# Optimization experiments

Measured on AMD Instinct MI355X. Metric: run time of the kernel, lower is better.

## Reference

```python
import jax, jax.numpy as jnp
import numpy as np

SEQ_LEN = 4096
EMBED_DIM = 2048
NUM_HEADS = 16
HEAD_DIM = EMBED_DIM // NUM_HEADS


def setup_inputs() -> dict:
    key = jax.random.key(0)
    k1, k2, k3 = jax.random.split(key, 3)
    x = jax.random.normal(k1, (SEQ_LEN, EMBED_DIM), dtype=jnp.float32)
    # Dense-layer params (lecun-normal-ish scaling for stability)
    W_qkv = jax.random.normal(k2, (EMBED_DIM, 3 * EMBED_DIM), dtype=jnp.float32) / np.sqrt(EMBED_DIM)
    b_qkv = jnp.zeros((3 * EMBED_DIM,), dtype=jnp.float32)
    W_out = jax.random.normal(k3, (EMBED_DIM, EMBED_DIM), dtype=jnp.float32) / np.sqrt(EMBED_DIM)
    b_out = jnp.zeros((EMBED_DIM,), dtype=jnp.float32)
    return {"x": x, "W_qkv": W_qkv, "b_qkv": b_qkv, "W_out": W_out, "b_out": b_out}


def reference(x, W_qkv, b_qkv, W_out, b_out):
    seq_len = x.shape[0]
    qkv = x @ W_qkv + b_qkv                       # (S, 3E)
    qkv = qkv.reshape(seq_len, 3, NUM_HEADS, HEAD_DIM)
    q, k, v = qkv[:, 0], qkv[:, 1], qkv[:, 2]     # each (S, H, D)
    scale = 1.0 / jnp.sqrt(jnp.float32(HEAD_DIM))
    # NOTE: faithful to source -- contracts over BOTH heads and head_dim,
    # producing a single (S, S) attention matrix shared across heads.
    attn = jnp.einsum('thd,shd->ts', q, k) * scale
    causal = jnp.triu(jnp.ones((seq_len, seq_len), dtype=bool), k=1)
    attn = jnp.where(causal, -jnp.inf, attn)
    attn = jax.nn.softmax(attn, axis=-1)
    out = jnp.einsum('ts,shd->thd', attn, v)      # (S, H, D)
    out = out.reshape(seq_len, EMBED_DIM)
    return out @ W_out + b_out
```

## Files before the change

### kernel.cpp

```cpp
#include <hip/hip_runtime.h>
#include <cstdint>
#include <cstddef>

#define SEQLEN 4096
#define EMBED  2048
#define NH     16
#define HD     128
#define N3     6144
#define SCALE  0.08838834764831845f
#define MBIAS  25.0f
#define LB3    12288
#define LB1    8192

typedef __attribute__((ext_vector_type(8))) short bf16x8;
typedef __attribute__((ext_vector_type(4))) float f32x4;
typedef unsigned short u16;

#define MFMA(a, b, c) __builtin_amdgcn_mfma_f32_16x16x32_bf16((a), (b), (c), 0, 0, 0)

__device__ inline u16 f2bf(float f) {
  uint32_t u = __float_as_uint(f);
  u += 0x7FFF + ((u >> 16) & 1);
  return (u16)(u >> 16);
}

__device__ inline float bf2f(u16 u) {
  return __uint_as_float(((uint32_t)u) << 16);
}

__device__ inline void gload_lds16(const u16* g, u16* l) {
  __builtin_amdgcn_global_load_lds((const __attribute__((address_space(1))) void*)g,
                                   (__attribute__((address_space(3))) void*)l, 16, 0, 0);
}

__device__ __forceinline__ void stage3(const u16* a0, const u16* a1, const u16* b0,
                                       u16* base, int w, int lane) {
  gload_lds16(a0, base + w * 512 + lane * 8);
  gload_lds16(a1, base + 4096 + w * 512 + lane * 8);
  gload_lds16(b0, base + 8192 + w * 512 + lane * 8);
}

__device__ __forceinline__ void mm256x128(const u16* gA, size_t sA, const u16* gB, size_t sB,
                                          int NT, u16* lds, f32x4 (&acc)[4][4]) {
  int tid = threadIdx.x;
  int w = tid >> 6, lane = tid & 63;
  int g = lane >> 4, lr = lane & 15;
  int wm = w >> 1, wn = w & 1;
  int arow = (w << 4) + (lane >> 2);
  int cb = (((lane & 3) ^ (arow & 3)) << 3);
  const u16* a0 = gA + (size_t)arow * sA + cb;
  const u16* a1 = a0 + (size_t)128 * sA;
  const u16* b0 = gB + (size_t)arow * sB + cb;
  int gx = ((g ^ (lr & 3)) << 3);
  int aoff = ((wm << 6) + lr) * 32 + gx;
  int boff = 8192 + ((wn << 6) + lr) * 32 + gx;
  stage3(a0, a1, b0, lds, w, lane);
  stage3(a0 + 32, a1 + 32, b0 + 32, lds + LB3, w, lane);
  asm volatile("s_waitcnt vmcnt(3)" ::: "memory");
  __builtin_amdgcn_s_barrier();
  for (int t = 0; t < NT; ++t) {
    u16* base = lds + (t % 3) * LB3;
    bf16x8 af[4], bfr[4];
    #pragma unroll
    for (int m = 0; m < 4; m++) af[m] = *(const bf16x8*)(base + aoff + m * 512);
    #pragma unroll
    for (int n = 0; n < 4; n++) bfr[n] = *(const bf16x8*)(base + boff + n * 512);
    if (t + 2 < NT) {
      int kt = (t + 2) << 5;
      stage3(a0 + kt, a1 + kt, b0 + kt, lds + ((t + 2) % 3) * LB3, w, lane);
    }
    __builtin_amdgcn_s_setprio(1);
    #pragma unroll
    for (int m = 0; m < 4; m++)
      #pragma unroll
      for (int n = 0; n < 4; n++)
        acc[m][n] = MFMA(af[m], bfr[n], acc[m][n]);
    __builtin_amdgcn_s_setprio(0);
    if (t + 1 < NT) {
      if (t + 2 < NT) asm volatile("s_waitcnt vmcnt(3)" ::: "memory");
      else            asm volatile("s_waitcnt vmcnt(0)" ::: "memory");
      __builtin_amdgcn_s_barrier();
    }
  }
  asm volatile("" ::: "memory");
}

__device__ __forceinline__ void stage2h(const u16* a0, const u16* b0, u16* base, int w, int lane) {
  gload_lds16(a0, base + w * 512 + lane * 8);
  gload_lds16(b0, base + 4096 + w * 512 + lane * 8);
}

__device__ __forceinline__ void mm128x128(const u16* gA, size_t sA, const u16* gB, size_t sB,
                                          int NT, u16* lds, f32x4 (&acc)[4][2]) {
  int tid = threadIdx.x;
  int w = tid >> 6, lane = tid & 63;
  int g = lane >> 4, lr = lane & 15;
  int wm = w >> 2, wn = w & 3;
  int srow = lane >> 2;
  int cb = (((lane & 3) ^ (srow & 3)) << 3);
  const u16* a0 = gA + (size_t)((w << 4) + srow) * sA + cb;
  const u16* b0 = gB + (size_t)((w << 4) + srow) * sB + cb;
  int gx = ((g ^ (lr & 3)) << 3);
  int aoff = ((wm << 6) + lr) * 32 + gx;
  int boff = 4096 + ((wn << 5) + lr) * 32 + gx;
  stage2h(a0, b0, lds, w, lane);
  stage2h(a0 + 32, b0 + 32, lds + LB1, w, lane);
  asm volatile("s_waitcnt vmcnt(2)" ::: "memory");
  __builtin_amdgcn_s_barrier();
  for (int t = 0; t < NT; ++t) {
    u16* base = lds + (t % 3) * LB1;
    bf16x8 af[4], bfr[2];
    #pragma unroll
    for (int m = 0; m < 4; m++) af[m] = *(const bf16x8*)(base + aoff + m * 512);
    #pragma unroll
    for (int n = 0; n < 2; n++) bfr[n] = *(const bf16x8*)(base + boff + n * 512);
    if (t + 2 < NT) {
      int kt = (t + 2) << 5;
      stage2h(a0 + kt, b0 + kt, lds + ((t + 2) % 3) * LB1, w, lane);
    }
    __builtin_amdgcn_s_setprio(1);
    #pragma unroll
    for (int m = 0; m < 4; m++)
      #pragma unroll
      for (int n = 0; n < 2; n++)
        acc[m][n] = MFMA(af[m], bfr[n], acc[m][n]);
    __builtin_amdgcn_s_setprio(0);
    if (t + 1 < NT) {
      if (t + 2 < NT) asm volatile("s_waitcnt vmcnt(2)" ::: "memory");
      else            asm volatile("s_waitcnt vmcnt(0)" ::: "memory");
      __builtin_amdgcn_s_barrier();
    }
  }
  asm volatile("" ::: "memory");
}

__global__ __launch_bounds__(256) void conv_f32_bf16(const float* __restrict__ in,
                                                     u16* __restrict__ out, int n) {
  int i = (blockIdx.x * 256 + threadIdx.x) * 4;
  if (i >= n) return;
  float4 v = *(const float4*)(in + i);
  ushort4 o;
  o.x = f2bf(v.x); o.y = f2bf(v.y); o.z = f2bf(v.z); o.w = f2bf(v.w);
  *(ushort4*)(out + i) = o;
}

__global__ __launch_bounds__(256) void transpose_conv(const float* __restrict__ in,
                                                      u16* __restrict__ out, int R, int C) {
  __shared__ float t[32][33];
  int c0 = blockIdx.x * 32, r0 = blockIdx.y * 32;
  int tx = threadIdx.x, ty = threadIdx.y;
  #pragma unroll
  for (int i = ty; i < 32; i += 8)
    t[i][tx] = in[(size_t)(r0 + i) * C + c0 + tx];
  __syncthreads();
  #pragma unroll
  for (int i = ty; i < 32; i += 8)
    out[(size_t)(c0 + i) * R + r0 + tx] = f2bf(t[tx][i]);
}

__global__ __launch_bounds__(256) void vtrans(const u16* __restrict__ qkv, u16* __restrict__ vT) {
  __shared__ u16 t[32][33];
  int c0 = blockIdx.x * 32, t0 = blockIdx.y * 32;
  int tx = threadIdx.x, ty = threadIdx.y;
  #pragma unroll
  for (int i = ty; i < 32; i += 8)
    t[i][tx] = qkv[(size_t)(t0 + i) * N3 + 2 * EMBED + c0 + tx];
  __syncthreads();
  #pragma unroll
  for (int i = ty; i < 32; i += 8)
    vT[(size_t)(c0 + i) * SEQLEN + t0 + tx] = t[tx][i];
}

__global__ __launch_bounds__(512, 4) void gemm_bt2(const u16* __restrict__ A, const u16* __restrict__ Bt,
                                                   const float* __restrict__ bias,
                                                   u16* __restrict__ Cb, float* __restrict__ Cf,
                                                   int M, int N, int K, int out_f32) {
  __shared__ __align__(16) u16 lds[3 * LB3];
  int bn = blockIdx.x, bm = blockIdx.y;
  f32x4 acc[4][4] = {};
  mm256x128(A + (size_t)(bm * 256) * K, K, Bt + (size_t)(bn * 128) * K, K, K >> 5, lds, acc);
  int tid = threadIdx.x;
  int w = tid >> 6, lane = tid & 63, g = lane >> 4, lr = lane & 15;
  int wm = w >> 1, wn = w & 1;
  int r0 = bm * 256 + wm * 64, c0 = bn * 128 + wn * 64;
  #pragma unroll
  for (int n = 0; n < 4; n++) {
    int c = c0 + n * 16 + lr;
    float bv = bias[c];
    #pragma unroll
    for (int m = 0; m < 4; m++)
      #pragma unroll
      for (int j = 0; j < 4; j++) {
        int r = r0 + m * 16 + g * 4 + j;
        float v = acc[m][n][j] + bv;
        if (out_f32) Cf[(size_t)r * N + c] = v;
        else         Cb[(size_t)r * N + c] = f2bf(v);
      }
  }
}

__global__ __launch_bounds__(512, 4) void sgemm_p2(const u16* __restrict__ qkv,
                                                   u16* __restrict__ P) {
  int bx = blockIdx.x, by = blockIdx.y;
  int r0g = by * 256, c0g = bx * 128;
  if (c0g > r0g + 255) return;
  __shared__ __align__(16) u16 lds[3 * LB3];
  f32x4 acc[4][4] = {};
  mm256x128(qkv + (size_t)r0g * N3, N3, qkv + (size_t)c0g * N3 + EMBED, N3, EMBED >> 5, lds, acc);
  int tid = threadIdx.x;
  int w = tid >> 6, lane = tid & 63, g = lane >> 4, lr = lane & 15;
  int wm = w >> 1, wn = w & 1;
  int r0 = r0g + wm * 64, c0 = c0g + wn * 64;
  #pragma unroll
  for (int m = 0; m < 4; m++)
    #pragma unroll
    for (int n = 0; n < 4; n++) {
      int c = c0 + n * 16 + lr;
      #pragma unroll
      for (int j = 0; j < 4; j++) {
        int r = r0 + m * 16 + g * 4 + j;
        float p = (c <= r) ? __expf(fmaf(acc[m][n][j], SCALE, -MBIAS)) : 0.f;
        P[(size_t)r * SEQLEN + c] = f2bf(p);
      }
    }
}

__global__ __launch_bounds__(256) void psum(const u16* __restrict__ P, float* __restrict__ L) {
  int wave = threadIdx.x >> 6, lane = threadIdx.x & 63;
  int r = blockIdx.x * 4 + wave;
  int ctop = ((r >> 8) + 1) * 256;
  const u16* Prow = P + (size_t)r * SEQLEN;
  float s = 0.f;
  for (int c = lane * 8; c < ctop; c += 512) {
    bf16x8 v = *(const bf16x8*)(Prow + c);
    #pragma unroll
    for (int j = 0; j < 8; j++) s += bf2f((u16)v[j]);
  }
  s += __shfl_xor(s, 1);  s += __shfl_xor(s, 2);  s += __shfl_xor(s, 4);
  s += __shfl_xor(s, 8);  s += __shfl_xor(s, 16); s += __shfl_xor(s, 32);
  if (lane == 0) L[r] = s;
}

__global__ __launch_bounds__(512, 4) void pv_gemm3(const u16* __restrict__ P,
                                                   const u16* __restrict__ vT,
                                                   const float* __restrict__ L,
                                                   u16* __restrict__ O) {
  __shared__ __align__(16) u16 lds[3 * LB1];
  int bx = blockIdx.x, pp = blockIdx.y;
  int tid = threadIdx.x;
  int w = tid >> 6, lane = tid & 63, g = lane >> 4, lr = lane & 15;
  int wm = w >> 2, wn = w & 3;
  int c0g = bx * 128;
  #pragma unroll
  for (int pass = 0; pass < 2; pass++) {
    int rt = pass ? pp : (31 - pp);
    int r0g = rt * 128;
    int NT = (r0g + 128) >> 5;
    f32x4 acc[4][2] = {};
    mm128x128(P + (size_t)r0g * SEQLEN, SEQLEN, vT + (size_t)c0g * SEQLEN, SEQLEN, NT, lds, acc);
    int r0 = r0g + wm * 64, c0 = c0g + wn * 32;
    #pragma unroll
    for (int m = 0; m < 4; m++) {
      float invl[4];
      #pragma unroll
      for (int j = 0; j < 4; j++)
        invl[j] = 1.f / L[r0 + m * 16 + g * 4 + j];
      #pragma unroll
      for (int n = 0; n < 2; n++) {
        int c = c0 + n * 16 + lr;
        #pragma unroll
        for (int j = 0; j < 4; j++) {
          int r = r0 + m * 16 + g * 4 + j;
          O[(size_t)r * EMBED + c] = f2bf(acc[m][n][j] * invl[j]);
        }
      }
    }
    __syncthreads();
  }
}

extern "C" void kernel_launch(void* const* d_in, const int* in_sizes, int n_in,
                              void* d_out, int out_size, void* d_ws, size_t ws_size,
                              hipStream_t stream) {
  const float* x     = (const float*)d_in[0];
  const float* W_qkv = (const float*)d_in[1];
  const float* b_qkv = (const float*)d_in[2];
  const float* W_out = (const float*)d_in[3];
  const float* b_out = (const float*)d_in[4];
  float* out = (float*)d_out;

  u16* xb    = (u16*)d_ws;
  u16* qkvb  = xb + (size_t)SEQLEN * EMBED;
  u16* Pbuf  = qkvb + (size_t)SEQLEN * N3;
  u16* vT    = Pbuf + (size_t)SEQLEN * SEQLEN;
  float* Lbuf = (float*)(vT + (size_t)EMBED * SEQLEN);
  u16* attb  = xb;
  u16* WqkvT = Pbuf;
  u16* WoutT = Pbuf;

  conv_f32_bf16<<<SEQLEN * EMBED / 1024, 256, 0, stream>>>(x, xb, SEQLEN * EMBED);
  transpose_conv<<<dim3(N3 / 32, EMBED / 32), dim3(32, 8), 0, stream>>>(W_qkv, WqkvT, EMBED, N3);
  gemm_bt2<<<dim3(N3 / 128, SEQLEN / 256), 512, 0, stream>>>(xb, WqkvT, b_qkv, qkvb, nullptr,
                                                             SEQLEN, N3, EMBED, 0);
  vtrans<<<dim3(EMBED / 32, SEQLEN / 32), dim3(32, 8), 0, stream>>>(qkvb, vT);
  sgemm_p2<<<dim3(SEQLEN / 128, SEQLEN / 256), 512, 0, stream>>>(qkvb, Pbuf);
  psum<<<SEQLEN / 4, 256, 0, stream>>>(Pbuf, Lbuf);
  pv_gemm3<<<dim3(EMBED / 128, 16), 512, 0, stream>>>(Pbuf, vT, Lbuf, attb);
  transpose_conv<<<dim3(EMBED / 32, EMBED / 32), dim3(32, 8), 0, stream>>>(W_out, WoutT, EMBED, EMBED);
  gemm_bt2<<<dim3(EMBED / 128, SEQLEN / 256), 512, 0, stream>>>(attb, WoutT, b_out, nullptr, out,
                                                                SEQLEN, EMBED, EMBED, 1);
}
```

Before: 318.2 us.

## Use 4-wave 256x128 GEMM tiles and fuse softmax row sums into score kernel

Adds a 256-thread GEMM mainloop in which each wave computes a 128x64 sub-tile (8x4 MFMA accumulators), giving more register reuse per LDS load. The QKV projection and the score kernel both use it. The score kernel also reduces exp values per row in registers and writes partial sums to a small buffer. A tiny kernel then sums those partials, replacing the pass that re-read the whole P matrix. The trade-offs are higher register pressure with fewer waves per block, plus an added memset and partial-sum buffer.

```diff
diff --git a/kernel.cpp b/kernel.cpp
--- a/kernel.cpp
+++ b/kernel.cpp
@@ -10,6 +10,7 @@
 #define SCALE  0.08838834764831845f
 #define MBIAS  25.0f
 #define LB3    12288
+#define LB4    12288
 #define LB1    8192
 
 typedef __attribute__((ext_vector_type(8))) short bf16x8;
@@ -78,6 +79,65 @@
     __builtin_amdgcn_s_setprio(0);
     if (t + 1 < NT) {
       if (t + 2 < NT) asm volatile("s_waitcnt vmcnt(3)" ::: "memory");
+      else            asm volatile("s_waitcnt vmcnt(0)" ::: "memory");
+      __builtin_amdgcn_s_barrier();
+    }
+  }
+  asm volatile("" ::: "memory");
+}
+
+__device__ __forceinline__ void stage6(const u16* a0, const u16* a1, const u16* a2, const u16* a3,
+                                       const u16* b0, const u16* b1, u16* base, int w, int lane) {
+  gload_lds16(a0, base + w * 512 + lane * 8);
+  gload_lds16(a1, base + 2048 + w * 512 + lane * 8);
+  gload_lds16(a2, base + 4096 + w * 512 + lane * 8);
+  gload_lds16(a3, base + 6144 + w * 512 + lane * 8);
+  gload_lds16(b0, base + 8192 + w * 512 + lane * 8);
+  gload_lds16(b1, base + 10240 + w * 512 + lane * 8);
+}
+
+__device__ __forceinline__ void mm256x128w4(const u16* gA, size_t sA, const u16* gB, size_t sB,
+                                            int NT, u16* lds, f32x4 (&acc)[8][4]) {
+  int tid = threadIdx.x;
+  int w = tid >> 6, lane = tid & 63;
+  int g = lane >> 4, lr = lane & 15;
+  int wm = w >> 1, wn = w & 1;
+  int arow = (w << 4) + (lane >> 2);
+  int cb = (((lane & 3) ^ (arow & 3)) << 3);
+  const u16* a0 = gA + (size_t)arow * sA + cb;
+  const u16* a1 = a0 + (size_t)64 * sA;
+  const u16* a2 = a0 + (size_t)128 * sA;
+  const u16* a3 = a0 + (size_t)192 * sA;
+  const u16* b0 = gB + (size_t)arow * sB + cb;
+  const u16* b1 = b0 + (size_t)64 * sB;
+  int gx = ((g ^ (lr & 3)) << 3);
+  int aoff = ((wm << 7) + lr) * 32 + gx;
+  int boff = 8192 + ((wn << 6) + lr) * 32 + gx;
+  stage6(a0, a1, a2, a3, b0, b1, lds, w, lane);
+  stage6(a0 + 32, a1 + 32, a2 + 32, a3 + 32, b0 + 32, b1 + 32, lds + LB4, w, lane);
+  asm volatile("s_waitcnt vmcnt(6)" ::: "memory");
+  __builtin_amdgcn_s_barrier();
+  for (int t = 0; t < NT; ++t) {
+    u16* base = lds + (t % 3) * LB4;
+    bf16x8 af[8], bfr[4];
+    #pragma unroll
+    for (int m = 0; m < 8; m++) af[m] = *(const bf16x8*)(base + aoff + m * 512);
+    #pragma unroll
+    for (int n = 0; n < 4; n++) bfr[n] = *(const bf16x8*)(base + boff + n * 512);
+    if (t + 2 < NT) {
+      int kt = (t + 2) << 5;
+      stage6(a0 + kt, a1 + kt, a2 + kt, a3 + kt, b0 + kt, b1 + kt,
+             lds + ((t + 2) % 3) * LB4, w, lane);
+    }
+    __builtin_amdgcn_s_setprio(1);
+    #pragma unroll
+    for (int m = 0; m < 8; m++)
+      #pragma unroll
+      for (int n = 0; n < 4; n++)
+        acc[m][n] = MFMA(af[m], bfr[n], acc[m][n]);
+    __builtin_amdgcn_s_setprio(0);
+    if (t + 1 < NT) {
+      if (t + 2 < NT) asm volatile("s_waitcnt vmcnt(6)" ::: "memory");
       else            asm volatile("s_waitcnt vmcnt(0)" ::: "memory");
       __builtin_amdgcn_s_barrier();
     }
@@ -171,10 +231,34 @@
     vT[(size_t)(c0 + i) * SEQLEN + t0 + tx] = t[tx][i];
 }
 
+__global__ __launch_bounds__(256, 2) void gemm_bt4(const u16* __restrict__ A, const u16* __restrict__ Bt,
+                                                   const float* __restrict__ bias,
+                                                   u16* __restrict__ Cb, int N, int K) {
+  __shared__ __align__(16) u16 lds[3 * LB4];
+  int bn = blockIdx.x, bm = blockIdx.y;
+  f32x4 acc[8][4] = {};
+  mm256x128w4(A + (size_t)(bm * 256) * K, K, Bt + (size_t)(bn * 128) * K, K, K >> 5, lds, acc);
+  int tid = threadIdx.x;
+  int w = tid >> 6, lane = tid & 63, g = lane >> 4, lr = lane & 15;
+  int wm = w >> 1, wn = w & 1;
+  int r0 = bm * 256 + wm * 128, c0 = bn * 128 + wn * 64;
+  #pragma unroll
+  for (int n = 0; n < 4; n++) {
+    int c = c0 + n * 16 + lr;
+    float bv = bias[c];
+    #pragma unroll
+    for (int m = 0; m < 8; m++)
+      #pragma unroll
+      for (int j = 0; j < 4; j++) {
+        int r = r0 + m * 16 + g * 4 + j;
+        Cb[(size_t)r * N + c] = f2bf(acc[m][n][j] + bv);
+      }
+  }
+}
+
 __global__ __launch_bounds__(512, 4) void gemm_bt2(const u16* __restrict__ A, const u16* __restrict__ Bt,
                                                    const float* __restrict__ bias,
-                                                   u16* __restrict__ Cb, float* __restrict__ Cf,
-                                                   int M, int N, int K, int out_f32) {
+                                                   float* __restrict__ Cf, int N, int K) {
   __shared__ __align__(16) u16 lds[3 * LB3];
   int bn = blockIdx.x, bm = blockIdx.y;
   f32x4 acc[4][4] = {};
@@ -192,50 +276,49 @@
       #pragma unroll
       for (int j = 0; j < 4; j++) {
         int r = r0 + m * 16 + g * 4 + j;
-        float v = acc[m][n][j] + bv;
-        if (out_f32) Cf[(size_t)r * N + c] = v;
-        else         Cb[(size_t)r * N + c] = f2bf(v);
+        Cf[(size_t)r * N + c] = acc[m][n][j] + bv;
       }
   }
 }
 
-__global__ __launch_bounds__(512, 4) void sgemm_p2(const u16* __restrict__ qkv,
-                                                   u16* __restrict__ P) {
+__global__ __launch_bounds__(256, 2) void sgemm_p4(const u16* __restrict__ qkv,
+                                                   u16* __restrict__ P,
+                                                   float* __restrict__ Lpart) {
   int bx = blockIdx.x, by = blockIdx.y;
   int r0g = by * 256, c0g = bx * 128;
   if (c0g > r0g + 255) return;
-  __shared__ __align__(16) u16 lds[3 * LB3];
-  f32x4 acc[4][4] = {};
-  mm256x128(qkv + (size_t)r0g * N3, N3, qkv + (size_t)c0g * N3 + EMBED, N3, EMBED >> 5, lds, acc);
+  __shared__ __align__(16) u16 lds[3 * LB4];
+  f32x4 acc[8][4] = {};
+  mm256x128w4(qkv + (size_t)r0g * N3, N3, qkv + (size_t)c0g * N3 + EMBED, N3, EMBED >> 5, lds, acc);
   int tid = threadIdx.x;
   int w = tid >> 6, lane = tid & 63, g = lane >> 4, lr = lane & 15;
   int wm = w >> 1, wn = w & 1;
-  int r0 = r0g + wm * 64, c0 = c0g + wn * 64;
-  #pragma unroll
-  for (int m = 0; m < 4; m++)
-    #pragma unroll
-    for (int n = 0; n < 4; n++) {
-      int c = c0 + n * 16 + lr;
-      #pragma unroll
-      for (int j = 0; j < 4; j++) {
-        int r = r0 + m * 16 + g * 4 + j;
+  int r0 = r0g + wm * 128, c0 = c0g + wn * 64;
+  int slot = bx * 2 + wn;
+  #pragma unroll
+  for (int m = 0; m < 8; m++)
+    #pragma unroll
+    for (int j = 0; j < 4; j++) {
+      int r = r0 + m * 16 + g * 4 + j;
+      float psv = 0.f;
+      #pragma unroll
+      for (int n = 0; n < 4; n++) {
+        int c = c0 + n * 16 + lr;
         float p = (c <= r) ? __expf(fmaf(acc[m][n][j], SCALE, -MBIAS)) : 0.f;
         P[(size_t)r * SEQLEN + c] = f2bf(p);
+        psv += p;
       }
-    }
-}
-
-__global__ __launch_bounds__(256) void psum(const u16* __restrict__ P, float* __restrict__ L) {
+      psv += __shfl_xor(psv, 1);  psv += __shfl_xor(psv, 2);
+      psv += __shfl_xor(psv, 4);  psv += __shfl_xor(psv, 8);
+      if (lr == 0) Lpart[(size_t)r * 64 + slot] = psv;
+    }
+}
+
+__global__ __launch_bounds__(256) void psum_small(const float* __restrict__ Lpart,
+                                                  float* __restrict__ L) {
   int wave = threadIdx.x >> 6, lane = threadIdx.x & 63;
   int r = blockIdx.x * 4 + wave;
-  int ctop = ((r >> 8) + 1) * 256;
-  const u16* Prow = P + (size_t)r * SEQLEN;
-  float s = 0.f;
-  for (int c = lane * 8; c < ctop; c += 512) {
-    bf16x8 v = *(const bf16x8*)(Prow + c);
-    #pragma unroll
-    for (int j = 0; j < 8; j++) s += bf2f((u16)v[j]);
-  }
+  float s = Lpart[(size_t)r * 64 + lane];
   s += __shfl_xor(s, 1);  s += __shfl_xor(s, 2);  s += __shfl_xor(s, 4);
   s += __shfl_xor(s, 8);  s += __shfl_xor(s, 16); s += __shfl_xor(s, 32);
   if (lane == 0) L[r] = s;
@@ -297,16 +380,16 @@
   u16* attb  = xb;
   u16* WqkvT = Pbuf;
   u16* WoutT = Pbuf;
+  float* Lpart = (float*)xb;
 
   conv_f32_bf16<<<SEQLEN * EMBED / 1024, 256, 0, stream>>>(x, xb, SEQLEN * EMBED);
   transpose_conv<<<dim3(N3 / 32, EMBED / 32), dim3(32, 8), 0, stream>>>(W_qkv, WqkvT, EMBED, N3);
-  gemm_bt2<<<dim3(N3 / 128, SEQLEN / 256), 512, 0, stream>>>(xb, WqkvT, b_qkv, qkvb, nullptr,
-                                                             SEQLEN, N3, EMBED, 0);
+  gemm_bt4<<<dim3(N3 / 128, SEQLEN / 256), 256, 0, stream>>>(xb, WqkvT, b_qkv, qkvb, N3, EMBED);
   vtrans<<<dim3(EMBED / 32, SEQLEN / 32), dim3(32, 8), 0, stream>>>(qkvb, vT);
-  sgemm_p2<<<dim3(SEQLEN / 128, SEQLEN / 256), 512, 0, stream>>>(qkvb, Pbuf);
-  psum<<<SEQLEN / 4, 256, 0, stream>>>(Pbuf, Lbuf);
+  hipMemsetAsync(Lpart, 0, (size_t)SEQLEN * 64 * sizeof(float), stream);
+  sgemm_p4<<<dim3(SEQLEN / 128, SEQLEN / 256), 256, 0, stream>>>(qkvb, Pbuf, Lpart);
+  psum_small<<<SEQLEN / 4, 256, 0, stream>>>(Lpart, Lbuf);
   pv_gemm3<<<dim3(EMBED / 128, 16), 512, 0, stream>>>(Pbuf, vT, Lbuf, attb);
   transpose_conv<<<dim3(EMBED / 32, EMBED / 32), dim3(32, 8), 0, stream>>>(W_out, WoutT, EMBED, EMBED);
-  gemm_bt2<<<dim3(EMBED / 128, SEQLEN / 256), 512, 0, stream>>>(attb, WoutT, b_out, nullptr, out,
-                                                                SEQLEN, EMBED, EMBED, 1);
-}
+  gemm_bt2<<<dim3(EMBED / 128, SEQLEN / 256), 512, 0, stream>>>(attb, WoutT, b_out, out, EMBED, EMBED);
+}
```

Result: no change. 320.7 us (+0.8%).
